# Kernel optimization log

Measured on AMD Instinct MI355X. Metric: run time of the kernel, lower is better.

The kernel has to match this reference:

```python
import jax, jax.numpy as jnp
import numpy as np

# Camera model constants (expected-value camera: gain multiply + baseline offset)
GAIN = 2.0
BASELINE = 100.0

B, E = 32, 64          # frames, emitters per frame
H = W = 128            # image size
R = 13                 # PSF ROI (patch) size
D = 32                 # number of z slices in the spline table


def setup_inputs() -> dict:
    key = jax.random.key(0)
    k1, k2, k3, k4 = jax.random.split(key, 4)
    # subpixel emitter positions: x in [0,W), y in [0,H), z in voxel units [0, D-1)
    u = jax.random.uniform(k1, (B, E, 3), dtype=jnp.float32)
    xyz = u * jnp.array([W, H, D - 1], dtype=jnp.float32)
    n_photons = 1000.0 + 4000.0 * jax.random.uniform(k2, (B, E), dtype=jnp.float32)
    bg = 10.0 + 90.0 * jax.random.uniform(k3, (B, H, W), dtype=jnp.float32)
    # cubic-spline coefficient table: [z_slice, roi_y, roi_x, 4(dz),4(dy),4(dx)]
    coeff = 0.01 * jax.random.normal(k4, (D, R, R, 4, 4, 4), dtype=jnp.float32)
    return {"xyz": xyz, "n_photons": n_photons, "bg": bg, "coeff": coeff}


def reference(xyz, n_photons, bg, coeff):
    Bb, Hh, Ww = bg.shape
    Dd, Rr = coeff.shape[0], coeff.shape[1]
    half = Rr // 2
    pow4 = jnp.arange(4)

    def render_one(pos, nph):
        x, y, z = pos[0], pos[1], pos[2]
        xf, yf = jnp.floor(x), jnp.floor(y)
        dx, dy = x - xf, y - yf
        zc = jnp.clip(z, 0.0, Dd - 1.0 - 1e-6)
        zf = jnp.floor(zc)
        zi = zf.astype(jnp.int32)
        dz = zc - zf
        px = dx ** pow4  # [4]
        py = dy ** pow4
        pz = dz ** pow4
        c = coeff[zi]  # [R,R,4,4,4] gather of this emitter's z-slice
        patch = jnp.einsum('yxabc,a,b,c->yx', c, pz, py, px) * nph  # [R,R]
        r0 = yf.astype(jnp.int32) - half
        c0 = xf.astype(jnp.int32) - half
        rows = r0 + jnp.arange(Rr)
        cols = c0 + jnp.arange(Rr)
        img = jnp.zeros((Hh, Ww), patch.dtype)
        # irregular scatter-add of the PSF patch; OOB (incl. negative) dropped
        return img.at[rows[:, None], cols[None, :]].add(patch, mode='drop')

    imgs = jax.vmap(jax.vmap(render_one))(xyz, n_photons)  # [B,E,H,W]
    y = imgs + bg[:, None]          # add background per frame
    return y * GAIN + BASELINE      # camera gain
```

## Files before the change

kernel.cpp:

```cpp
#include <hip/hip_runtime.h>

constexpr int   B = 32, E = 64, H = 128, W = 128, R = 13, D = 32;
constexpr float GAIN = 2.0f, BASELINE = 100.0f;
constexpr int   HALF = R / 2;
constexpr int   PLANE = H * W;

__device__ __forceinline__ float pw(float v, int p) {
    float r = 1.0f;
    if (p >= 1) r = v;
    if (p >= 2) r *= v;
    if (p >= 3) r *= v;
    return r;
}

__device__ __forceinline__ int patch_idx(int c, int o) {
    int p = c - o;
    if (p >= 0 && p < R) return p;
    p = c - o - 128;
    if (p >= 0 && p < R) return p;
    return -1;
}

__global__ __launch_bounds__(256)
void render_kernel(const float* __restrict__ xyz,
                   const float* __restrict__ n_photons,
                   const float* __restrict__ bg,
                   const float* __restrict__ coeff,
                   float* __restrict__ out)
{
    const int be = blockIdx.x;
    const int b  = be >> 6;
    const int tid = threadIdx.x;

    __shared__ float s_w[64];
    __shared__ float s_patch[R * R];

    const float x = xyz[be * 3 + 0];
    const float y = xyz[be * 3 + 1];
    const float z = xyz[be * 3 + 2];
    const float nph = n_photons[be];

    const float xf = floorf(x), yf = floorf(y);
    const float dx = x - xf,   dy = y - yf;
    float zc = fminf(fmaxf(z, 0.0f), (float)(D - 1) - 1e-6f);
    const float zf = floorf(zc);
    const int   zi = (int)zf;
    const float dz = zc - zf;

    const int r0 = (int)yf - HALF;
    const int c0 = (int)xf - HALF;

    if (tid < 64) {
        const int a = tid >> 4;
        const int bb = (tid >> 2) & 3;
        const int c = tid & 3;
        s_w[tid] = pw(dz, a) * pw(dy, bb) * pw(dx, c);
    }
    __syncthreads();

    if (tid < R * R) {
        const int prow = tid / R;
        const int pcol = tid - prow * R;
        const float* cp = coeff + (((size_t)zi * R + prow) * R + pcol) * 64;
        float acc = 0.0f;
        #pragma unroll
        for (int k = 0; k < 64; k += 4) {
            const float4 cc = *(const float4*)(cp + k);
            acc += cc.x * s_w[k + 0];
            acc += cc.y * s_w[k + 1];
            acc += cc.z * s_w[k + 2];
            acc += cc.w * s_w[k + 3];
        }
        s_patch[tid] = acc * nph;
    }
    __syncthreads();

    const float* __restrict__ bgp  = bg  + (size_t)b  * PLANE;
    float*       __restrict__ outp = out + (size_t)be * PLANE;

    #pragma unroll
    for (int i = tid; i < PLANE / 4; i += 256) {
        const int pix = i << 2;
        const int row = pix >> 7;
        const int col = pix & (W - 1);
        float4 v = *(const float4*)(bgp + pix);

        const int pr = patch_idx(row, r0);
        if (pr >= 0) {
            const float* prow = s_patch + pr * R;
            const int p0 = patch_idx(col + 0, c0);
            const int p1 = patch_idx(col + 1, c0);
            const int p2 = patch_idx(col + 2, c0);
            const int p3 = patch_idx(col + 3, c0);
            if (p0 >= 0) v.x += prow[p0];
            if (p1 >= 0) v.y += prow[p1];
            if (p2 >= 0) v.z += prow[p2];
            if (p3 >= 0) v.w += prow[p3];
        }

        v.x = v.x * GAIN + BASELINE;
        v.y = v.y * GAIN + BASELINE;
        v.z = v.z * GAIN + BASELINE;
        v.w = v.w * GAIN + BASELINE;
        *(float4*)(outp + pix) = v;
    }
}

extern "C" void kernel_launch(void* const* d_in, const int* in_sizes, int n_in,
                              void* d_out, int out_size, void* d_ws, size_t ws_size,
                              hipStream_t stream) {
    const float* xyz       = (const float*)d_in[0];
    const float* n_photons = (const float*)d_in[1];
    const float* bg        = (const float*)d_in[2];
    const float* coeff     = (const float*)d_in[3];
    float* out = (float*)d_out;

    render_kernel<<<dim3(B * E), dim3(256), 0, stream>>>(xyz, n_photons, bg, coeff, out);
}
```

Baseline: 171.9 us.

## Split render into bulk background stream kernel and sparse patch overwrite kernel

Replaces the single fused kernel with two. The first streams gain*bg+baseline into all B*E output planes as plain float4 copies with no patch-index branching. The second computes each 13x13 PSF patch and overwrites only the affected pixels with (bg+patch)*gain+baseline. The aim is to strip the per-pixel patch checks out of the bandwidth-bound loop. The cost is an extra launch and a small second pass of scattered writes over memory already written, and correctness relies on the launch order on one stream.

```diff
diff --git a/kernel.cpp b/kernel.cpp
--- a/kernel.cpp
+++ b/kernel.cpp
@@ -4,6 +4,7 @@
 constexpr float GAIN = 2.0f, BASELINE = 100.0f;
 constexpr int   HALF = R / 2;
 constexpr int   PLANE = H * W;
+constexpr int   PLANE4 = PLANE / 4;
 
 __device__ __forceinline__ float pw(float v, int p) {
     float r = 1.0f;
@@ -13,27 +14,39 @@
     return r;
 }
 
-__device__ __forceinline__ int patch_idx(int c, int o) {
-    int p = c - o;
-    if (p >= 0 && p < R) return p;
-    p = c - o - 128;
-    if (p >= 0 && p < R) return p;
-    return -1;
+__global__ __launch_bounds__(256)
+void stream_bg_kernel(const float* __restrict__ bg,
+                      float* __restrict__ out)
+{
+    const int tid = threadIdx.x;
+    const long long base4 = (long long)blockIdx.x * 1024;
+    #pragma unroll
+    for (int j = 0; j < 4; ++j) {
+        const long long idx4 = base4 + j * 256 + tid;
+        const int within4 = (int)(idx4 & (PLANE4 - 1));
+        const int b       = (int)(idx4 >> 18);
+        const float4 v = *(const float4*)(bg + ((size_t)b << 14) + ((size_t)within4 << 2));
+        float4 o;
+        o.x = v.x * GAIN + BASELINE;
+        o.y = v.y * GAIN + BASELINE;
+        o.z = v.z * GAIN + BASELINE;
+        o.w = v.w * GAIN + BASELINE;
+        *(float4*)(out + (idx4 << 2)) = o;
+    }
 }
 
 __global__ __launch_bounds__(256)
-void render_kernel(const float* __restrict__ xyz,
-                   const float* __restrict__ n_photons,
-                   const float* __restrict__ bg,
-                   const float* __restrict__ coeff,
-                   float* __restrict__ out)
+void patch_kernel(const float* __restrict__ xyz,
+                  const float* __restrict__ n_photons,
+                  const float* __restrict__ bg,
+                  const float* __restrict__ coeff,
+                  float* __restrict__ out)
 {
-    const int be = blockIdx.x;
-    const int b  = be >> 6;
+    const int be  = blockIdx.x;
+    const int b   = be >> 6;
     const int tid = threadIdx.x;
 
     __shared__ float s_w[64];
-    __shared__ float s_patch[R * R];
 
     const float x = xyz[be * 3 + 0];
     const float y = xyz[be * 3 + 1];
@@ -51,17 +64,18 @@
     const int c0 = (int)xf - HALF;
 
     if (tid < 64) {
-        const int a = tid >> 4;
+        const int a  = tid >> 4;
         const int bb = (tid >> 2) & 3;
-        const int c = tid & 3;
+        const int c  = tid & 3;
         s_w[tid] = pw(dz, a) * pw(dy, bb) * pw(dx, c);
     }
     __syncthreads();
 
     if (tid < R * R) {
-        const int prow = tid / R;
-        const int pcol = tid - prow * R;
-        const float* cp = coeff + (((size_t)zi * R + prow) * R + pcol) * 64;
+        const int pr = tid / R;
+        const int pc = tid - pr * R;
+
+        const float* cp = coeff + (((size_t)zi * R + pr) * R + pc) * 64;
         float acc = 0.0f;
         #pragma unroll
         for (int k = 0; k < 64; k += 4) {
@@ -71,38 +85,15 @@
             acc += cc.z * s_w[k + 2];
             acc += cc.w * s_w[k + 3];
         }
-        s_patch[tid] = acc * nph;
-    }
-    __syncthreads();
+        const float patch = acc * nph;
 
-    const float* __restrict__ bgp  = bg  + (size_t)b  * PLANE;
-    float*       __restrict__ outp = out + (size_t)be * PLANE;
-
-    #pragma unroll
-    for (int i = tid; i < PLANE / 4; i += 256) {
-        const int pix = i << 2;
-        const int row = pix >> 7;
-        const int col = pix & (W - 1);
-        float4 v = *(const float4*)(bgp + pix);
-
-        const int pr = patch_idx(row, r0);
-        if (pr >= 0) {
-            const float* prow = s_patch + pr * R;
-            const int p0 = patch_idx(col + 0, c0);
-            const int p1 = patch_idx(col + 1, c0);
-            const int p2 = patch_idx(col + 2, c0);
-            const int p3 = patch_idx(col + 3, c0);
-            if (p0 >= 0) v.x += prow[p0];
-            if (p1 >= 0) v.y += prow[p1];
-            if (p2 >= 0) v.z += prow[p2];
-            if (p3 >= 0) v.w += prow[p3];
+        int row = r0 + pr;  if (row < 0) row += H;
+        int col = c0 + pc;  if (col < 0) col += W;
+        if (row < H && col < W) {
+            const size_t ppix = ((size_t)(row << 7)) + col;
+            const float  bgv  = bg[((size_t)b << 14) + ppix];
+            out[((size_t)be << 14) + ppix] = (bgv + patch) * GAIN + BASELINE;
         }
-
-        v.x = v.x * GAIN + BASELINE;
-        v.y = v.y * GAIN + BASELINE;
-        v.z = v.z * GAIN + BASELINE;
-        v.w = v.w * GAIN + BASELINE;
-        *(float4*)(outp + pix) = v;
     }
 }
 
@@ -115,5 +106,6 @@
     const float* coeff     = (const float*)d_in[3];
     float* out = (float*)d_out;
 
-    render_kernel<<<dim3(B * E), dim3(256), 0, stream>>>(xyz, n_photons, bg, coeff, out);
+    stream_bg_kernel<<<dim3(8192), dim3(256), 0, stream>>>(bg, out);
+    patch_kernel<<<dim3(B * E), dim3(256), 0, stream>>>(xyz, n_photons, bg, coeff, out);
 }
```

Result: faster. 161.7 us (-5.9%).
